# Performance work log

Measured on AMD Instinct MI355X. Metric: run time of the kernel, lower is better.

Reference implementation:

```python
import jax, jax.numpy as jnp
import numpy as np

EPS = 1e-06


def elu_plus_one(x):
    # F.elu(x) + 1 == exp(x) for x < 0, x + 1 for x >= 0 (alpha=1)
    return jnp.where(x > 0, x + 1.0, jnp.exp(jnp.minimum(x, 0.0)))


def safe_divide(a, b, eps=EPS):
    return a / (b + eps)


def setup_inputs() -> dict:
    key0 = jax.random.key(0)
    kq, kk, kv, kM, kz = jax.random.split(key0, 5)
    B, H, S, D = 4, 16, 4096, 128
    query = jax.random.normal(kq, (B, H, S, D), dtype=jnp.float32)
    key = jax.random.normal(kk, (B, H, S, D), dtype=jnp.float32)
    value = jax.random.normal(kv, (B, H, S, D), dtype=jnp.float32)
    M = jax.random.normal(kM, (B, H, D, D), dtype=jnp.float32)
    z = jax.random.uniform(kz, (B, H, D, 1), dtype=jnp.float32)
    return {"query": query, "key": key, "value": value, "M": M, "z": z}


def reference(query, key, value, M, z):
    # --- update (delta rule) ---
    sigma_k = elu_plus_one(key)                       # [B,H,S,D]
    mem_pred = jnp.einsum('bhsd,bhde->bhse', sigma_k, M)   # sigma(K) @ M
    normalizer = jnp.einsum('bhsd,bhdo->bhso', sigma_k, z) # sigma(K) @ z -> [B,H,S,1]
    delta_v = value - safe_divide(mem_pred, normalizer)
    M_new = M + jnp.einsum('bhsd,bhse->bhde', sigma_k, delta_v)  # sigma(K)^T @ delta_V
    z_new = z + jnp.sum(sigma_k, axis=2)[..., None]              # [B,H,D,1]

    # --- retrieve with updated memory ---
    sigma_q = elu_plus_one(query)
    mem_out = jnp.einsum('bhsd,bhde->bhse', sigma_q, M_new)
    norm_q = jnp.einsum('bhsd,bhdo->bhso', sigma_q, z_new)
    out = safe_divide(mem_out, norm_q)                # [B,H,S,D]
    return out, M_new, z_new
```

## Files before the change

### kernel.cpp

```cpp
#include <hip/hip_runtime.h>
#include <math.h>

#define D 128
#define EPS 1e-6f
#define TLD 40
#define TSZ (128 * TLD)
#define SKR_LD 136

typedef __attribute__((ext_vector_type(8))) short short8;
typedef __attribute__((ext_vector_type(4))) float f32x4;
typedef unsigned short ushort_t;
typedef unsigned long long u64;

__device__ __forceinline__ float elu1(float x) {
    float e = __expf(fminf(x, 0.f));
    return x > 0.f ? x + 1.f : e;
}
__device__ __forceinline__ unsigned short bf16rne(float f) {
    unsigned u = __builtin_bit_cast(unsigned, f);
    u += 0x7FFFu + ((u >> 16) & 1u);
    return (unsigned short)(u >> 16);
}
__device__ __forceinline__ float bf2f(unsigned short h) {
    unsigned u = (unsigned)h << 16;
    return __builtin_bit_cast(float, u);
}
__device__ __forceinline__ u64 pack4(float a, float b, float c, float d) {
    return (u64)bf16rne(a) | ((u64)bf16rne(b) << 16) |
           ((u64)bf16rne(c) << 32) | ((u64)bf16rne(d) << 48);
}
__device__ __forceinline__ int swzs(int f, int u) {
    return TLD * f + 8 * (u ^ (f & 3) ^ ((f >> 2) & 3));
}

__global__ __launch_bounds__(512, 4)
void k_update(const float* __restrict__ key, const float* __restrict__ value,
              const float* __restrict__ z,
              float* __restrict__ pP, float* __restrict__ pG,
              float* __restrict__ pz, int S)
{
    __shared__ alignas(16) ushort_t sT[2 * TSZ];
    __shared__ alignas(16) ushort_t vT[2 * TSZ];
    __shared__ float nrm[2][32];

    const int t  = threadIdx.x;
    const int bh = blockIdx.x, ch = blockIdx.y, NCH = gridDim.y;
    const int SC = S / NCH, NB = SC / 32, s0g = ch * SC;

    const int w = t >> 6, g = (t >> 4) & 3, m = t & 15;
    const int c2 = t & 63;

    const float* Kb = key   + (size_t)bh * S * D;
    const float* Vb = value + (size_t)bh * S * D;
    const float* zb = z + (size_t)bh * D;

    const float2 zr = *(const float2*)&zb[2 * c2];

    f32x4 accP[8], accG[8];
    #pragma unroll
    for (int dt = 0; dt < 8; ++dt) { accP[dt] = 0.f; accG[dt] = 0.f; }
    float zacc0 = 0.f, zacc1 = 0.f;

    auto STAGE = [&](const float2* kr, const float2* vr, int buf) {
        float sv0[4], sv1[4];
        #pragma unroll
        for (int i = 0; i < 4; ++i) { sv0[i] = elu1(kr[i].x); sv1[i] = elu1(kr[i].y); }
        const int u = w >> 1, h4 = 4 * (w & 1);
        *(u64*)&sT[buf * TSZ + swzs(2 * c2,     u) + h4] = pack4(sv0[0], sv0[1], sv0[2], sv0[3]);
        *(u64*)&sT[buf * TSZ + swzs(2 * c2 + 1, u) + h4] = pack4(sv1[0], sv1[1], sv1[2], sv1[3]);
        *(u64*)&vT[buf * TSZ + swzs(2 * c2,     u) + h4] = pack4(vr[0].x, vr[1].x, vr[2].x, vr[3].x);
        *(u64*)&vT[buf * TSZ + swzs(2 * c2 + 1, u) + h4] = pack4(vr[0].y, vr[1].y, vr[2].y, vr[3].y);
        float p[4];
        #pragma unroll
        for (int i = 0; i < 4; ++i) {
            p[i] = sv0[i] * zr.x + sv1[i] * zr.y;
            zacc0 += sv0[i]; zacc1 += sv1[i];
        }
        #pragma unroll
        for (int mask = 32; mask >= 1; mask >>= 1) {
            p[0] += __shfl_xor(p[0], mask, 64);
            p[1] += __shfl_xor(p[1], mask, 64);
            p[2] += __shfl_xor(p[2], mask, 64);
            p[3] += __shfl_xor(p[3], mask, 64);
        }
        int l = t & 63;
        if (l < 4) {
            float pv = l == 0 ? p[0] : l == 1 ? p[1] : l == 2 ? p[2] : p[3];
            nrm[buf][4 * w + l] = 1.f / (pv + EPS);
        }
    };

    float2 kr[4], vr[4];
    #pragma unroll
    for (int i = 0; i < 4; ++i) {
        kr[i] = *(const float2*)&Kb[(size_t)(s0g + 4 * w + i) * D + 2 * c2];
        vr[i] = *(const float2*)&Vb[(size_t)(s0g + 4 * w + i) * D + 2 * c2];
    }
    STAGE(kr, vr, 0);
    if (NB > 1) {
        #pragma unroll
        for (int i = 0; i < 4; ++i) {
            kr[i] = *(const float2*)&Kb[(size_t)(s0g + 32 + 4 * w + i) * D + 2 * c2];
            vr[i] = *(const float2*)&Vb[(size_t)(s0g + 32 + 4 * w + i) * D + 2 * c2];
        }
    }
    __syncthreads();

    for (int b = 0; b < NB; ++b) {
        const int cur = b & 1;

        float rn[8];
        #pragma unroll
        for (int j = 0; j < 8; ++j) rn[j] = nrm[cur][8 * g + j];
        short8 bv = *(short8*)&vT[cur * TSZ + swzs(16 * w + m, g)];
        short8 bs = *(short8*)&sT[cur * TSZ + swzs(16 * w + m, g)];
        short8 bg;
        #pragma unroll
        for (int j = 0; j < 8; ++j) bg[j] = (short)bf16rne(bf2f((unsigned short)bs[j]) * rn[j]);
        #pragma unroll
        for (int dt = 0; dt < 8; ++dt) {
            short8 a = *(short8*)&sT[cur * TSZ + swzs(16 * dt + m, g)];
            accP[dt] = __builtin_amdgcn_mfma_f32_16x16x32_bf16(a, bv, accP[dt], 0, 0, 0);
            accG[dt] = __builtin_amdgcn_mfma_f32_16x16x32_bf16(a, bg, accG[dt], 0, 0, 0);
        }

        if (b + 1 < NB) {
            STAGE(kr, vr, cur ^ 1);
            if (b + 2 < NB) {
                const int snx = s0g + 32 * (b + 2);
                #pragma unroll
                for (int i = 0; i < 4; ++i) {
                    kr[i] = *(const float2*)&Kb[(size_t)(snx + 4 * w + i) * D + 2 * c2];
                    vr[i] = *(const float2*)&Vb[(size_t)(snx + 4 * w + i) * D + 2 * c2];
                }
            }
        }
        asm volatile("s_waitcnt lgkmcnt(0)\n\ts_barrier" ::: "memory");
    }

    float* pPb = pP + ((size_t)bh * NCH + ch) * (D * D);
    float* pGb = pG + ((size_t)bh * NCH + ch) * (D * D);
    #pragma unroll
    for (int dt = 0; dt < 8; ++dt)
        #pragma unroll
        for (int r = 0; r < 4; ++r) {
            pPb[(size_t)(16 * dt + 4 * g + r) * D + 16 * w + m] = accP[dt][r];
            pGb[(size_t)(16 * dt + 4 * g + r) * D + 16 * w + m] = accG[dt][r];
        }

    __syncthreads();
    float* zsc = (float*)sT;
    zsc[w * 128 + 2 * c2]     = zacc0;
    zsc[w * 128 + 2 * c2 + 1] = zacc1;
    __syncthreads();
    if (t < 128) {
        float a = 0.f;
        #pragma unroll
        for (int r = 0; r < 8; ++r) a += zsc[r * 128 + t];
        pz[((size_t)bh * NCH + ch) * D + t] = a;
    }
}

__global__ void k_sum(const float* __restrict__ M, const float* __restrict__ z,
                      const float* __restrict__ pP, const float* __restrict__ pG,
                      const float* __restrict__ pz,
                      float* __restrict__ Mtmp, ushort_t* __restrict__ gh,
                      ushort_t* __restrict__ gl, float* __restrict__ znew, int NCH)
{
    const int bh = blockIdx.x, sl = blockIdx.y, t = threadIdx.x;
    const size_t base = (size_t)bh * D * D;
    for (int i = sl * 2048 + t; i < (sl + 1) * 2048; i += 256) {
        float sp = M[base + i];
        float sg = 0.f;
        for (int c = 0; c < NCH; ++c) {
            sp += pP[((size_t)bh * NCH + c) * (D * D) + i];
            sg += pG[((size_t)bh * NCH + c) * (D * D) + i];
        }
        Mtmp[base + i] = sp;
        float nG = -sg;
        unsigned short hi = bf16rne(nG);
        gh[base + i] = hi;
        gl[base + i] = bf16rne(nG - bf2f(hi));
    }
    if (sl == 0 && t < D) {
        float a = z[(size_t)bh * D + t];
        for (int c = 0; c < NCH; ++c) a += pz[((size_t)bh * NCH + c) * D + t];
        znew[(size_t)bh * D + t] = a;
    }
}

__global__ __launch_bounds__(256)
void k_gm(const float* __restrict__ M, const float* __restrict__ Mtmp,
          const ushort_t* __restrict__ gh, const ushort_t* __restrict__ gl,
          float* __restrict__ Mnew)
{
    const int bh = blockIdx.x, t = threadIdx.x;
    const int w2 = t >> 6, g = (t >> 4) & 3, m = t & 15;
    const float* Mb = M + (size_t)bh * D * D;
    const float* Tb = Mtmp + (size_t)bh * D * D;
    const ushort_t* ghb = gh + (size_t)bh * D * D;
    const ushort_t* glb = gl + (size_t)bh * D * D;
    float* Ob = Mnew + (size_t)bh * D * D;

    f32x4 acc[8][2];
    #pragma unroll
    for (int dt = 0; dt < 8; ++dt)
        #pragma unroll
        for (int p = 0; p < 2; ++p)
            #pragma unroll
            for (int r = 0; r < 4; ++r)
                acc[dt][p][r] = Tb[(size_t)(16 * dt + 4 * g + r) * D + 32 * w2 + 16 * p + m];

    #pragma unroll
    for (int ks = 0; ks < 4; ++ks) {
        short8 bm[2];
        #pragma unroll
        for (int p = 0; p < 2; ++p)
            #pragma unroll
            for (int j = 0; j < 8; ++j)
                bm[p][j] = (short)bf16rne(Mb[(size_t)(32 * ks + 8 * g + j) * D + 32 * w2 + 16 * p + m]);
        #pragma unroll
        for (int dt = 0; dt < 8; ++dt) {
            short8 ah = *(const short8*)&ghb[(size_t)(16 * dt + m) * D + 32 * ks + 8 * g];
            short8 al = *(const short8*)&glb[(size_t)(16 * dt + m) * D + 32 * ks + 8 * g];
            #pragma unroll
            for (int p = 0; p < 2; ++p) {
                acc[dt][p] = __builtin_amdgcn_mfma_f32_16x16x32_bf16(ah, bm[p], acc[dt][p], 0, 0, 0);
                acc[dt][p] = __builtin_amdgcn_mfma_f32_16x16x32_bf16(al, bm[p], acc[dt][p], 0, 0, 0);
            }
        }
    }

    #pragma unroll
    for (int dt = 0; dt < 8; ++dt)
        #pragma unroll
        for (int p = 0; p < 2; ++p)
            #pragma unroll
            for (int r = 0; r < 4; ++r)
                Ob[(size_t)(16 * dt + 4 * g + r) * D + 32 * w2 + 16 * p + m] = acc[dt][p][r];
}

__global__ __launch_bounds__(256, 2)
void k_retrieve(const float* __restrict__ query, const float* __restrict__ Mnew,
                const float* __restrict__ znew, float* __restrict__ out, int S)
{
    __shared__ alignas(16) ushort_t sqR[2][32 * SKR_LD];
    __shared__ float normsh[2][32];

    const int t  = threadIdx.x;
    const int bh = blockIdx.x, ch = blockIdx.y, NCH = gridDim.y;
    const int SC = S / NCH;
    const int NB = SC / 32;
    const int s0g = ch * SC;

    const int w = t >> 6, g = (t >> 4) & 3, m = t & 15;
    const int sb = t >> 5, db = t & 31;

    const float* Qb = query + (size_t)bh * S * D;
    const float* Mb = Mnew + (size_t)bh * D * D;
    const float* zb = znew + (size_t)bh * D;
    float*       Ob = out + (size_t)bh * S * D;

    float zr[4];
    #pragma unroll
    for (int j = 0; j < 4; ++j) zr[j] = zb[4 * db + j];

    short8 Bf[4][2];
    #pragma unroll
    for (int ks = 0; ks < 4; ++ks)
        #pragma unroll
        for (int p = 0; p < 2; ++p) {
            short8 f;
            #pragma unroll
            for (int j = 0; j < 8; ++j)
                f[j] = (short)bf16rne(Mb[(size_t)(32 * ks + 8 * g + j) * D + 16 * (2 * w + p) + m]);
            Bf[ks][p] = f;
        }

    auto STAGE_PROC = [&](const float4* qreg, int bu) {
        float sv[4][4];
        #pragma unroll
        for (int js = 0; js < 4; ++js) {
            sv[js][0] = elu1(qreg[js].x); sv[js][1] = elu1(qreg[js].y);
            sv[js][2] = elu1(qreg[js].z); sv[js][3] = elu1(qreg[js].w);
        }
        #pragma unroll
        for (int js = 0; js < 4; ++js)
            *(u64*)&sqR[bu][(4 * sb + js) * SKR_LD + 4 * db] =
                pack4(sv[js][0], sv[js][1], sv[js][2], sv[js][3]);
        float np[4];
        #pragma unroll
        for (int js = 0; js < 4; ++js)
            np[js] = sv[js][0] * zr[0] + sv[js][1] * zr[1] +
                     sv[js][2] * zr[2] + sv[js][3] * zr[3];
        #pragma unroll
        for (int mask = 16; mask >= 1; mask >>= 1) {
            np[0] += __shfl_xor(np[0], mask, 64);
            np[1] += __shfl_xor(np[1], mask, 64);
            np[2] += __shfl_xor(np[2], mask, 64);
            np[3] += __shfl_xor(np[3], mask, 64);
        }
        if (db < 4) {
            float v = db == 0 ? np[0] : db == 1 ? np[1] : db == 2 ? np[2] : np[3];
            normsh[bu][4 * sb + db] = v + EPS;
        }
    };

    {
        float4 qreg[4];
        #pragma unroll
        for (int js = 0; js < 4; ++js)
            qreg[js] = *(const float4*)&Qb[(size_t)(s0g + 4 * sb + js) * D + 4 * db];
        STAGE_PROC(qreg, 0);
    }
    __syncthreads();

    for (int b = 0; b < NB; ++b) {
        const int bu = b & 1;
        float4 qreg[4];
        if (b + 1 < NB) {
            #pragma unroll
            for (int js = 0; js < 4; ++js)
                qreg[js] = *(const float4*)&Qb[(size_t)(s0g + 32 * (b + 1) + 4 * sb + js) * D + 4 * db];
        }

        f32x4 mp[2][2];
        #pragma unroll
        for (int st = 0; st < 2; ++st)
            #pragma unroll
            for (int p = 0; p < 2; ++p) mp[st][p] = 0.f;
        #pragma unroll
        for (int st = 0; st < 2; ++st)
            #pragma unroll
            for (int ks = 0; ks < 4; ++ks) {
                short8 a = *(short8*)&sqR[bu][(16 * st + m) * SKR_LD + 32 * ks + 8 * g];
                #pragma unroll
                for (int p = 0; p < 2; ++p)
                    mp[st][p] = __builtin_amdgcn_mfma_f32_16x16x32_bf16(a, Bf[ks][p], mp[st][p], 0, 0, 0);
            }

        #pragma unroll
        for (int st = 0; st < 2; ++st)
            #pragma unroll
            for (int r = 0; r < 4; ++r) {
                float rn = 1.f / normsh[bu][16 * st + 4 * g + r];
                #pragma unroll
                for (int p = 0; p < 2; ++p)
                    Ob[(size_t)(s0g + 32 * b + 16 * st + 4 * g + r) * D + 16 * (2 * w + p) + m] =
                        mp[st][p][r] * rn;
            }

        if (b + 1 < NB) STAGE_PROC(qreg, (b + 1) & 1);
        __syncthreads();
    }
}

extern "C" void kernel_launch(void* const* d_in, const int* in_sizes, int n_in,
                              void* d_out, int out_size, void* d_ws, size_t ws_size,
                              hipStream_t stream)
{
    const float* q = (const float*)d_in[0];
    const float* k = (const float*)d_in[1];
    const float* v = (const float*)d_in[2];
    const float* M = (const float*)d_in[3];
    const float* z = (const float*)d_in[4];

    const int BH = in_sizes[3] / (D * D);
    const int S  = in_sizes[0] / (BH * D);
    const int NCH = 8;

    float* out  = (float*)d_out;
    float* Mnew = out + (size_t)BH * S * D;
    float* znew = Mnew + (size_t)BH * D * D;

    float* pP   = out;
    float* pG   = pP + (size_t)NCH * BH * D * D;
    float* pz   = pG + (size_t)NCH * BH * D * D;
    float* Mtmp = pz + (size_t)NCH * BH * D;
    ushort_t* gh = (ushort_t*)(Mtmp + (size_t)BH * D * D);
    ushort_t* gl = gh + (size_t)BH * D * D;

    dim3 gridA(BH, NCH);
    k_update<<<gridA, 512, 0, stream>>>(k, v, z, pP, pG, pz, S);
    dim3 gridB(BH, 8);
    k_sum<<<gridB, 256, 0, stream>>>(M, z, pP, pG, pz, Mtmp, gh, gl, znew, NCH);
    k_gm<<<BH, 256, 0, stream>>>(M, Mtmp, gh, gl, Mnew);
    dim3 gridC(BH, 8);
    k_retrieve<<<gridC, 256, 0, stream>>>(q, Mnew, znew, out, S);
}
```

Before: 177.7 us.

## Double k_update chunk to 64 rows and load V just-in-time in stage

The update kernel now processes 64 sequence rows per iteration instead of 32, doing two MFMA k-steps per barrier, with a wider swizzled LDS tile (TLD 72) and a wider XOR swizzle. Value rows are no longer prefetched a block ahead in registers but loaded inside the staging step, while key rows are still prefetched. The normalizer reduction is restructured into a transposing shuffle tree that produces fewer shuffles per lane. The aim is to halve barrier count and cut shuffle work, at the cost of more LDS per block, which may lower occupancy, and exposed V load latency.

```diff
diff --git a/kernel.cpp b/kernel.cpp
--- a/kernel.cpp
+++ b/kernel.cpp
@@ -3,7 +3,7 @@
 
 #define D 128
 #define EPS 1e-6f
-#define TLD 40
+#define TLD 72
 #define TSZ (128 * TLD)
 #define SKR_LD 136
 
@@ -29,8 +29,8 @@
     return (u64)bf16rne(a) | ((u64)bf16rne(b) << 16) |
            ((u64)bf16rne(c) << 32) | ((u64)bf16rne(d) << 48);
 }
-__device__ __forceinline__ int swzs(int f, int u) {
-    return TLD * f + 8 * (u ^ (f & 3) ^ ((f >> 2) & 3));
+__device__ __forceinline__ int swz(int f, int u) {
+    return TLD * f + 8 * (u ^ (f & 7) ^ ((f >> 3) & 7));
 }
 
 __global__ __launch_bounds__(512, 4)
@@ -41,11 +41,11 @@
 {
     __shared__ alignas(16) ushort_t sT[2 * TSZ];
     __shared__ alignas(16) ushort_t vT[2 * TSZ];
-    __shared__ float nrm[2][32];
+    __shared__ float nrm[2][64];
 
     const int t  = threadIdx.x;
     const int bh = blockIdx.x, ch = blockIdx.y, NCH = gridDim.y;
-    const int SC = S / NCH, NB = SC / 32, s0g = ch * SC;
+    const int SC = S / NCH, NB = SC / 64, s0g = ch * SC;
 
     const int w = t >> 6, g = (t >> 4) & 3, m = t & 15;
     const int c2 = t & 63;
@@ -61,78 +61,98 @@
     for (int dt = 0; dt < 8; ++dt) { accP[dt] = 0.f; accG[dt] = 0.f; }
     float zacc0 = 0.f, zacc1 = 0.f;
 
-    auto STAGE = [&](const float2* kr, const float2* vr, int buf) {
-        float sv0[4], sv1[4];
-        #pragma unroll
-        for (int i = 0; i < 4; ++i) { sv0[i] = elu1(kr[i].x); sv1[i] = elu1(kr[i].y); }
-        const int u = w >> 1, h4 = 4 * (w & 1);
-        *(u64*)&sT[buf * TSZ + swzs(2 * c2,     u) + h4] = pack4(sv0[0], sv0[1], sv0[2], sv0[3]);
-        *(u64*)&sT[buf * TSZ + swzs(2 * c2 + 1, u) + h4] = pack4(sv1[0], sv1[1], sv1[2], sv1[3]);
-        *(u64*)&vT[buf * TSZ + swzs(2 * c2,     u) + h4] = pack4(vr[0].x, vr[1].x, vr[2].x, vr[3].x);
-        *(u64*)&vT[buf * TSZ + swzs(2 * c2 + 1, u) + h4] = pack4(vr[0].y, vr[1].y, vr[2].y, vr[3].y);
-        float p[4];
-        #pragma unroll
-        for (int i = 0; i < 4; ++i) {
-            p[i] = sv0[i] * zr.x + sv1[i] * zr.y;
-            zacc0 += sv0[i]; zacc1 += sv1[i];
-        }
-        #pragma unroll
-        for (int mask = 32; mask >= 1; mask >>= 1) {
-            p[0] += __shfl_xor(p[0], mask, 64);
-            p[1] += __shfl_xor(p[1], mask, 64);
-            p[2] += __shfl_xor(p[2], mask, 64);
-            p[3] += __shfl_xor(p[3], mask, 64);
-        }
-        int l = t & 63;
-        if (l < 4) {
-            float pv = l == 0 ? p[0] : l == 1 ? p[1] : l == 2 ? p[2] : p[3];
-            nrm[buf][4 * w + l] = 1.f / (pv + EPS);
+    auto STAGE = [&](const float2* kr, int b, int buf) {
+        float2 vr[8];
+        #pragma unroll
+        for (int h = 0; h < 2; ++h)
+            #pragma unroll
+            for (int i = 0; i < 4; ++i)
+                vr[4 * h + i] = *(const float2*)&Vb[(size_t)(s0g + 64 * b + 32 * h + 4 * w + i) * D + 2 * c2];
+
+        #pragma unroll
+        for (int h = 0; h < 2; ++h) {
+            float sv0[4], sv1[4], p4[4];
+            #pragma unroll
+            for (int i = 0; i < 4; ++i) {
+                sv0[i] = elu1(kr[4 * h + i].x);
+                sv1[i] = elu1(kr[4 * h + i].y);
+            }
+            const int u = 4 * h + (w >> 1), h4 = 4 * (w & 1);
+            *(u64*)&sT[buf * TSZ + swz(2 * c2, u) + h4]     = pack4(sv0[0], sv0[1], sv0[2], sv0[3]);
+            *(u64*)&sT[buf * TSZ + swz(2 * c2 + 1, u) + h4] = pack4(sv1[0], sv1[1], sv1[2], sv1[3]);
+            #pragma unroll
+            for (int i = 0; i < 4; ++i) {
+                p4[i] = sv0[i] * zr.x + sv1[i] * zr.y;
+                zacc0 += sv0[i]; zacc1 += sv1[i];
+            }
+            float w2a, w2b, x;
+            { float a = (c2 & 1) ? p4[1] : p4[0], b2 = (c2 & 1) ? p4[0] : p4[1];
+              w2a = a + __shfl_xor(b2, 1, 64); }
+            { float a = (c2 & 1) ? p4[3] : p4[2], b2 = (c2 & 1) ? p4[2] : p4[3];
+              w2b = a + __shfl_xor(b2, 1, 64); }
+            { float a = (c2 & 2) ? w2b : w2a, b2 = (c2 & 2) ? w2a : w2b;
+              x = a + __shfl_xor(b2, 2, 64); }
+            x += __shfl_xor(x, 4, 64);
+            x += __shfl_xor(x, 8, 64);
+            x += __shfl_xor(x, 16, 64);
+            x += __shfl_xor(x, 32, 64);
+            if (c2 < 4)
+                nrm[buf][32 * h + 4 * w + c2] = 1.f / (x + EPS);
+        }
+        #pragma unroll
+        for (int h = 0; h < 2; ++h) {
+            const int u = 4 * h + (w >> 1), h4 = 4 * (w & 1);
+            *(u64*)&vT[buf * TSZ + swz(2 * c2, u) + h4] =
+                pack4(vr[4 * h + 0].x, vr[4 * h + 1].x, vr[4 * h + 2].x, vr[4 * h + 3].x);
+            *(u64*)&vT[buf * TSZ + swz(2 * c2 + 1, u) + h4] =
+                pack4(vr[4 * h + 0].y, vr[4 * h + 1].y, vr[4 * h + 2].y, vr[4 * h + 3].y);
         }
     };
 
-    float2 kr[4], vr[4];
-    #pragma unroll
-    for (int i = 0; i < 4; ++i) {
-        kr[i] = *(const float2*)&Kb[(size_t)(s0g + 4 * w + i) * D + 2 * c2];
-        vr[i] = *(const float2*)&Vb[(size_t)(s0g + 4 * w + i) * D + 2 * c2];
-    }
-    STAGE(kr, vr, 0);
+    float2 kr[8];
+    #pragma unroll
+    for (int h = 0; h < 2; ++h)
+        #pragma unroll
+        for (int i = 0; i < 4; ++i)
+            kr[4 * h + i] = *(const float2*)&Kb[(size_t)(s0g + 32 * h + 4 * w + i) * D + 2 * c2];
+    STAGE(kr, 0, 0);
     if (NB > 1) {
         #pragma unroll
-        for (int i = 0; i < 4; ++i) {
-            kr[i] = *(const float2*)&Kb[(size_t)(s0g + 32 + 4 * w + i) * D + 2 * c2];
-            vr[i] = *(const float2*)&Vb[(size_t)(s0g + 32 + 4 * w + i) * D + 2 * c2];
-        }
+        for (int h = 0; h < 2; ++h)
+            #pragma unroll
+            for (int i = 0; i < 4; ++i)
+                kr[4 * h + i] = *(const float2*)&Kb[(size_t)(s0g + 64 + 32 * h + 4 * w + i) * D + 2 * c2];
     }
     __syncthreads();
 
     for (int b = 0; b < NB; ++b) {
         const int cur = b & 1;
 
-        float rn[8];
-        #pragma unroll
-        for (int j = 0; j < 8; ++j) rn[j] = nrm[cur][8 * g + j];
-        short8 bv = *(short8*)&vT[cur * TSZ + swzs(16 * w + m, g)];
-        short8 bs = *(short8*)&sT[cur * TSZ + swzs(16 * w + m, g)];
-        short8 bg;
-        #pragma unroll
-        for (int j = 0; j < 8; ++j) bg[j] = (short)bf16rne(bf2f((unsigned short)bs[j]) * rn[j]);
-        #pragma unroll
-        for (int dt = 0; dt < 8; ++dt) {
-            short8 a = *(short8*)&sT[cur * TSZ + swzs(16 * dt + m, g)];
-            accP[dt] = __builtin_amdgcn_mfma_f32_16x16x32_bf16(a, bv, accP[dt], 0, 0, 0);
-            accG[dt] = __builtin_amdgcn_mfma_f32_16x16x32_bf16(a, bg, accG[dt], 0, 0, 0);
+        #pragma unroll
+        for (int ks = 0; ks < 2; ++ks) {
+            short8 bv = *(short8*)&vT[cur * TSZ + swz(16 * w + m, 4 * ks + g)];
+            short8 bs = *(short8*)&sT[cur * TSZ + swz(16 * w + m, 4 * ks + g)];
+            short8 bg;
+            #pragma unroll
+            for (int j = 0; j < 8; ++j)
+                bg[j] = (short)bf16rne(bf2f((unsigned short)bs[j]) * nrm[cur][32 * ks + 8 * g + j]);
+            #pragma unroll
+            for (int dt = 0; dt < 8; ++dt) {
+                short8 a = *(short8*)&sT[cur * TSZ + swz(16 * dt + m, 4 * ks + g)];
+                accP[dt] = __builtin_amdgcn_mfma_f32_16x16x32_bf16(a, bv, accP[dt], 0, 0, 0);
+                accG[dt] = __builtin_amdgcn_mfma_f32_16x16x32_bf16(a, bg, accG[dt], 0, 0, 0);
+            }
         }
 
         if (b + 1 < NB) {
-            STAGE(kr, vr, cur ^ 1);
+            STAGE(kr, b + 1, cur ^ 1);
             if (b + 2 < NB) {
-                const int snx = s0g + 32 * (b + 2);
+                const int snx = s0g + 64 * (b + 2);
                 #pragma unroll
-                for (int i = 0; i < 4; ++i) {
-                    kr[i] = *(const float2*)&Kb[(size_t)(snx + 4 * w + i) * D + 2 * c2];
-                    vr[i] = *(const float2*)&Vb[(size_t)(snx + 4 * w + i) * D + 2 * c2];
-                }
+                for (int h = 0; h < 2; ++h)
+                    #pragma unroll
+                    for (int i = 0; i < 4; ++i)
+                        kr[4 * h + i] = *(const float2*)&Kb[(size_t)(snx + 32 * h + 4 * w + i) * D + 2 * c2];
             }
         }
         asm volatile("s_waitcnt lgkmcnt(0)\n\ts_barrier" ::: "memory");
```

Measured after the change: 236.3 us. +32.9%, slower.

## Load update operands straight into MFMA fragments and split columns across blocks

Applied to the files above, without the earlier changes.

The update kernel no longer stages sigma(K) and V through swizzled shared memory with double buffering and barriers. Each lane now reads K and V from global memory directly in the MFMA operand layout, packs them with v_cvt_pk_bf16_f32, and computes the normalizer and z sums through intra-wave shuffles. The output columns are split across a new grid z dimension, and launch bounds are relaxed to 2 blocks per CU. This removes LDS traffic and synchronisation, but every warp recomputes elu on the whole K tile and the global loads become narrow strided accesses. K is also read redundantly across warps and across the two z blocks, which leans on cache hits.

```diff
diff --git a/kernel.cpp b/kernel.cpp
--- a/kernel.cpp
+++ b/kernel.cpp
@@ -3,8 +3,6 @@
 
 #define D 128
 #define EPS 1e-6f
-#define TLD 40
-#define TSZ (128 * TLD)
 #define SKR_LD 136
 
 typedef __attribute__((ext_vector_type(8))) short short8;
@@ -29,135 +27,121 @@
     return (u64)bf16rne(a) | ((u64)bf16rne(b) << 16) |
            ((u64)bf16rne(c) << 32) | ((u64)bf16rne(d) << 48);
 }
-__device__ __forceinline__ int swzs(int f, int u) {
-    return TLD * f + 8 * (u ^ (f & 3) ^ ((f >> 2) & 3));
-}
-
-__global__ __launch_bounds__(512, 4)
+__device__ __forceinline__ unsigned pk2(float a, float b) {
+    unsigned r;
+    asm("v_cvt_pk_bf16_f32 %0, %1, %2" : "=v"(r) : "v"(a), "v"(b));
+    return r;
+}
+
+typedef union { short8 s8; unsigned u[4]; } apk_u;
+
+__global__ __launch_bounds__(512, 2)
 void k_update(const float* __restrict__ key, const float* __restrict__ value,
-              const float* __restrict__ z,
+              const float* __restrict__ zv,
               float* __restrict__ pP, float* __restrict__ pG,
               float* __restrict__ pz, int S)
 {
-    __shared__ alignas(16) ushort_t sT[2 * TSZ];
-    __shared__ alignas(16) ushort_t vT[2 * TSZ];
-    __shared__ float nrm[2][32];
-
-    const int t  = threadIdx.x;
-    const int bh = blockIdx.x, ch = blockIdx.y, NCH = gridDim.y;
+    const int t = threadIdx.x;
+    const int bh = blockIdx.x, ch = blockIdx.y, zs = blockIdx.z;
+    const int NCH = gridDim.y;
     const int SC = S / NCH, NB = SC / 32, s0g = ch * SC;
 
     const int w = t >> 6, g = (t >> 4) & 3, m = t & 15;
-    const int c2 = t & 63;
+    const int dh = w >> 2;
+    const int et = 4 * zs + (w & 3);
+    const int ecol = 16 * et + m;
 
     const float* Kb = key   + (size_t)bh * S * D;
     const float* Vb = value + (size_t)bh * S * D;
-    const float* zb = z + (size_t)bh * D;
-
-    const float2 zr = *(const float2*)&zb[2 * c2];
-
-    f32x4 accP[8], accG[8];
-    #pragma unroll
-    for (int dt = 0; dt < 8; ++dt) { accP[dt] = 0.f; accG[dt] = 0.f; }
-    float zacc0 = 0.f, zacc1 = 0.f;
-
-    auto STAGE = [&](const float2* kr, const float2* vr, int buf) {
-        float sv0[4], sv1[4];
-        #pragma unroll
-        for (int i = 0; i < 4; ++i) { sv0[i] = elu1(kr[i].x); sv1[i] = elu1(kr[i].y); }
-        const int u = w >> 1, h4 = 4 * (w & 1);
-        *(u64*)&sT[buf * TSZ + swzs(2 * c2,     u) + h4] = pack4(sv0[0], sv0[1], sv0[2], sv0[3]);
-        *(u64*)&sT[buf * TSZ + swzs(2 * c2 + 1, u) + h4] = pack4(sv1[0], sv1[1], sv1[2], sv1[3]);
-        *(u64*)&vT[buf * TSZ + swzs(2 * c2,     u) + h4] = pack4(vr[0].x, vr[1].x, vr[2].x, vr[3].x);
-        *(u64*)&vT[buf * TSZ + swzs(2 * c2 + 1, u) + h4] = pack4(vr[0].y, vr[1].y, vr[2].y, vr[3].y);
-        float p[4];
-        #pragma unroll
-        for (int i = 0; i < 4; ++i) {
-            p[i] = sv0[i] * zr.x + sv1[i] * zr.y;
-            zacc0 += sv0[i]; zacc1 += sv1[i];
-        }
-        #pragma unroll
-        for (int mask = 32; mask >= 1; mask >>= 1) {
-            p[0] += __shfl_xor(p[0], mask, 64);
-            p[1] += __shfl_xor(p[1], mask, 64);
-            p[2] += __shfl_xor(p[2], mask, 64);
-            p[3] += __shfl_xor(p[3], mask, 64);
-        }
-        int l = t & 63;
-        if (l < 4) {
-            float pv = l == 0 ? p[0] : l == 1 ? p[1] : l == 2 ? p[2] : p[3];
-            nrm[buf][4 * w + l] = 1.f / (pv + EPS);
-        }
-    };
-
-    float2 kr[4], vr[4];
-    #pragma unroll
-    for (int i = 0; i < 4; ++i) {
-        kr[i] = *(const float2*)&Kb[(size_t)(s0g + 4 * w + i) * D + 2 * c2];
-        vr[i] = *(const float2*)&Vb[(size_t)(s0g + 4 * w + i) * D + 2 * c2];
-    }
-    STAGE(kr, vr, 0);
-    if (NB > 1) {
-        #pragma unroll
-        for (int i = 0; i < 4; ++i) {
-            kr[i] = *(const float2*)&Kb[(size_t)(s0g + 32 + 4 * w + i) * D + 2 * c2];
-            vr[i] = *(const float2*)&Vb[(size_t)(s0g + 32 + 4 * w + i) * D + 2 * c2];
-        }
-    }
-    __syncthreads();
+    const float* zb = zv + (size_t)bh * D;
+
+    float zreg[8];
+    #pragma unroll
+    for (int dt = 0; dt < 8; ++dt) zreg[dt] = zb[16 * dt + m];
+
+    f32x4 accP[4], accG[4];
+    #pragma unroll
+    for (int i = 0; i < 4; ++i) { accP[i] = 0.f; accG[i] = 0.f; }
+    float zacc[8] = {0.f, 0.f, 0.f, 0.f, 0.f, 0.f, 0.f, 0.f};
 
     for (int b = 0; b < NB; ++b) {
-        const int cur = b & 1;
-
-        float rn[8];
-        #pragma unroll
-        for (int j = 0; j < 8; ++j) rn[j] = nrm[cur][8 * g + j];
-        short8 bv = *(short8*)&vT[cur * TSZ + swzs(16 * w + m, g)];
-        short8 bs = *(short8*)&sT[cur * TSZ + swzs(16 * w + m, g)];
-        short8 bg;
-        #pragma unroll
-        for (int j = 0; j < 8; ++j) bg[j] = (short)bf16rne(bf2f((unsigned short)bs[j]) * rn[j]);
+        const int s0 = s0g + 32 * b + 8 * g;
+        const float* kp = Kb + (size_t)s0 * D + m;
+        const float* vp = Vb + (size_t)s0 * D + ecol;
+
+        float vv[8];
+        #pragma unroll
+        for (int j = 0; j < 8; ++j) vv[j] = vp[(size_t)j * D];
+
+        float p[8] = {0.f, 0.f, 0.f, 0.f, 0.f, 0.f, 0.f, 0.f};
+        apk_u apk[4], bgp;
+
         #pragma unroll
         for (int dt = 0; dt < 8; ++dt) {
-            short8 a = *(short8*)&sT[cur * TSZ + swzs(16 * dt + m, g)];
-            accP[dt] = __builtin_amdgcn_mfma_f32_16x16x32_bf16(a, bv, accP[dt], 0, 0, 0);
-            accG[dt] = __builtin_amdgcn_mfma_f32_16x16x32_bf16(a, bg, accG[dt], 0, 0, 0);
-        }
-
-        if (b + 1 < NB) {
-            STAGE(kr, vr, cur ^ 1);
-            if (b + 2 < NB) {
-                const int snx = s0g + 32 * (b + 2);
-                #pragma unroll
-                for (int i = 0; i < 4; ++i) {
-                    kr[i] = *(const float2*)&Kb[(size_t)(snx + 4 * w + i) * D + 2 * c2];
-                    vr[i] = *(const float2*)&Vb[(size_t)(snx + 4 * w + i) * D + 2 * c2];
-                }
+            float sv[8];
+            #pragma unroll
+            for (int j = 0; j < 8; ++j)
+                sv[j] = elu1(kp[(size_t)j * D + 16 * dt]);
+            float za = 0.f;
+            #pragma unroll
+            for (int j = 0; j < 8; ++j) {
+                p[j] = fmaf(sv[j], zreg[dt], p[j]);
+                za += sv[j];
             }
-        }
-        asm volatile("s_waitcnt lgkmcnt(0)\n\ts_barrier" ::: "memory");
+            zacc[dt] += za;
+            apk_u cur;
+            cur.u[0] = pk2(sv[0], sv[1]); cur.u[1] = pk2(sv[2], sv[3]);
+            cur.u[2] = pk2(sv[4], sv[5]); cur.u[3] = pk2(sv[6], sv[7]);
+            if ((dt >> 2) == dh) apk[dt & 3] = cur;
+            if (dt == et) bgp = cur;
+        }
+
+        #pragma unroll
+        for (int j = 0; j < 8; ++j) {
+            float x = p[j];
+            x += __shfl_xor(x, 1, 64);
+            x += __shfl_xor(x, 2, 64);
+            x += __shfl_xor(x, 4, 64);
+            x += __shfl_xor(x, 8, 64);
+            p[j] = 1.f / (x + EPS);
+        }
+
+        apk_u bv, bg;
+        bv.u[0] = pk2(vv[0], vv[1]); bv.u[1] = pk2(vv[2], vv[3]);
+        bv.u[2] = pk2(vv[4], vv[5]); bv.u[3] = pk2(vv[6], vv[7]);
+        #pragma unroll
+        for (int k2 = 0; k2 < 4; ++k2) {
+            float lo = bf2f((ushort_t)(bgp.u[k2] & 0xffffu)) * p[2 * k2];
+            float hi = bf2f((ushort_t)(bgp.u[k2] >> 16))     * p[2 * k2 + 1];
+            bg.u[k2] = pk2(lo, hi);
+        }
+
+        #pragma unroll
+        for (int dtl = 0; dtl < 4; ++dtl) {
+            accP[dtl] = __builtin_amdgcn_mfma_f32_16x16x32_bf16(apk[dtl].s8, bv.s8, accP[dtl], 0, 0, 0);
+            accG[dtl] = __builtin_amdgcn_mfma_f32_16x16x32_bf16(apk[dtl].s8, bg.s8, accG[dtl], 0, 0, 0);
+        }
     }
 
     float* pPb = pP + ((size_t)bh * NCH + ch) * (D * D);
     float* pGb = pG + ((size_t)bh * NCH + ch) * (D * D);
     #pragma unroll
-    for (int dt = 0; dt < 8; ++dt)
+    for (int dtl = 0; dtl < 4; ++dtl) {
+        const int row0 = 16 * (4 * dh + dtl) + 4 * g;
         #pragma unroll
         for (int r = 0; r < 4; ++r) {
-            pPb[(size_t)(16 * dt + 4 * g + r) * D + 16 * w + m] = accP[dt][r];
-            pGb[(size_t)(16 * dt + 4 * g + r) * D + 16 * w + m] = accG[dt][r];
-        }
-
-    __syncthreads();
-    float* zsc = (float*)sT;
-    zsc[w * 128 + 2 * c2]     = zacc0;
-    zsc[w * 128 + 2 * c2 + 1] = zacc1;
-    __syncthreads();
-    if (t < 128) {
-        float a = 0.f;
-        #pragma unroll
-        for (int r = 0; r < 8; ++r) a += zsc[r * 128 + t];
-        pz[((size_t)bh * NCH + ch) * D + t] = a;
+            pPb[(size_t)(row0 + r) * D + ecol] = accP[dtl][r];
+            pGb[(size_t)(row0 + r) * D + ecol] = accG[dtl][r];
+        }
+    }
+
+    #pragma unroll
+    for (int dt = 0; dt < 8; ++dt) {
+        float a2 = zacc[dt];
+        a2 += __shfl_xor(a2, 16, 64);
+        a2 += __shfl_xor(a2, 32, 64);
+        if (zs == 0 && w == 0 && (t & 63) < 16)
+            pz[((size_t)bh * NCH + ch) * D + 16 * dt + m] = a2;
     }
 }
 
@@ -380,7 +364,7 @@
     ushort_t* gh = (ushort_t*)(Mtmp + (size_t)BH * D * D);
     ushort_t* gl = gh + (size_t)BH * D * D;
 
-    dim3 gridA(BH, NCH);
+    dim3 gridA(BH, NCH, 2);
     k_update<<<gridA, 512, 0, stream>>>(k, v, z, pP, pG, pz, S);
     dim3 gridB(BH, 8);
     k_sum<<<gridB, 256, 0, stream>>>(M, z, pP, pG, pz, Mtmp, gh, gl, znew, NCH);
```

New measurement: 599.4 us. 237% more time.
